# Kernel optimization log

Hardware: AMD Instinct MI355X
Metric: run time of the kernel (lower is better)

## Reference

```python
import jax, jax.numpy as jnp
import numpy as np

NUM_GROUP = 32
CHANNELS = 512
NUM_PER_GROUP = CHANNELS // NUM_GROUP  # 16
BN_EPS = 1e-5


def setup_inputs() -> dict:
    key = jax.random.key(0)
    k = jax.random.split(key, 5)
    B, C, W, H = 32, CHANNELS, 56, 56
    x = jax.random.normal(k[0], (B, C, W, H), dtype=jnp.float32)
    fc_w = jax.random.normal(k[1], (C, C), dtype=jnp.float32) / np.float32(np.sqrt(C))
    fc_b = jax.random.normal(k[2], (C,), dtype=jnp.float32) * 0.01
    bn_gamma = jnp.ones((C,), jnp.float32) + 0.1 * jax.random.normal(k[3], (C,), dtype=jnp.float32)
    bn_beta = 0.1 * jax.random.normal(k[4], (C,), dtype=jnp.float32)
    return {"x": x, "fc_w": fc_w, "fc_b": fc_b, "bn_gamma": bn_gamma, "bn_beta": bn_beta}


def reference(x, fc_w, fc_b, bn_gamma, bn_beta):
    b, c, w, h = x.shape
    G, P = NUM_GROUP, NUM_PER_GROUP
    # NHWC flatten -> [N, C], N = b*w*h
    t = x.transpose(0, 2, 3, 1).reshape(-1, c)
    t = t + (t @ fc_w.T + fc_b)                         # fc + residual
    t = t.reshape(-1, G, P)                             # [N, G, P]
    # bmm(t^T, t): [N, P, G] x [N, G, P] -> [N, P, P], then /32 and tanh
    s = jnp.tanh(jnp.einsum('ngp,ngq->npq', t, t) / 32.0)
    s = s.reshape(b, w, w, P * P)                       # requires w == h
    # F.interpolate(size=(w, c), mode='nearest') over last two dims:
    # dim-2 is w->w (identity); dim-3 is P*P -> c with src = floor(dst*in/out)
    idx = (jnp.arange(c) * (P * P)) // c
    s = s[..., idx]                                     # [b, w, w, c]
    s = s.transpose(0, 3, 1, 2)                         # [b, c, w, w]
    # BatchNorm2d, training-mode batch statistics (biased var), eps=1e-5
    mean = s.mean(axis=(0, 2, 3), keepdims=True)
    var = s.var(axis=(0, 2, 3), keepdims=True)
    s = (s - mean) * jax.lax.rsqrt(var + BN_EPS)
    s = s * bn_gamma[None, :, None, None] + bn_beta[None, :, None, None]
    return x + s
```

## Files before the change

kernel.cpp:

```cpp
#include <hip/hip_runtime.h>
#include <hip/hip_bf16.h>
#include <cstdint>

typedef __bf16 bf16x8 __attribute__((ext_vector_type(8)));
typedef unsigned short ushortx8 __attribute__((ext_vector_type(8)));
typedef unsigned short ushortx4 __attribute__((ext_vector_type(4)));
typedef float f32x4 __attribute__((ext_vector_type(4)));

constexpr int Cc  = 512;
constexpr int Ssp = 3136;
constexpr float NINV = 1.f / 100352.f;

__device__ __forceinline__ unsigned short f2bf(float f) {
    union { float f; unsigned u; } a; a.f = f;
    unsigned u = a.u;
    unsigned r = u + 0x7fffu + ((u >> 16) & 1u);
    return (unsigned short)(r >> 16);
}
__device__ __forceinline__ float bf2f(unsigned short h) {
    union { unsigned u; float f; } a; a.u = ((unsigned)h) << 16;
    return a.f;
}
__device__ __forceinline__ float tanh_fast(float u) {
    float e = __expf(2.f * u);
    return 1.f - 2.f / (e + 1.f);
}
__device__ __forceinline__ int swz(int row, int k) {
    return k ^ (((row >> 2) & 7) << 3);
}

__global__ void kWconv(const float* __restrict__ w, unsigned short* __restrict__ wb) {
    int i = (blockIdx.x * 256 + threadIdx.x) * 4;
    float4 v = *(const float4*)(w + i);
    ushortx4 o;
    o[0] = f2bf(v.x); o[1] = f2bf(v.y); o[2] = f2bf(v.z); o[3] = f2bf(v.w);
    *(ushortx4*)(wb + i) = o;
}

__global__ __launch_bounds__(512) void kA(
    const float* __restrict__ x, const unsigned short* __restrict__ wb,
    const float* __restrict__ fcb, float* __restrict__ sbuf,
    float* __restrict__ gstats)
{
    __shared__ __attribute__((aligned(16))) unsigned short xl[64 * 72];
    __shared__ __attribute__((aligned(16))) unsigned short tl[64 * 520];
    __shared__ float statsl[512];

    const int tid  = threadIdx.x;
    const int wave = tid >> 6;
    const int lane = tid & 63;
    const int lg   = lane >> 4;
    const int lm   = lane & 15;

    const int blk = blockIdx.x;
    const int b   = blk / 49;
    const int sc  = blk % 49;
    const float* xA = x + (size_t)b * Cc * Ssp + sc * 64;

    f32x4 acc[4][4];
#pragma unroll
    for (int mi = 0; mi < 4; ++mi)
#pragma unroll
        for (int ni = 0; ni < 4; ++ni) acc[mi][ni] = (f32x4){0.f, 0.f, 0.f, 0.f};

    float bias[4];
#pragma unroll
    for (int ni = 0; ni < 4; ++ni) bias[ni] = fcb[wave * 64 + ni * 16 + lm];

    const int stid = tid >> 4;
    const int s4   = (tid & 15) * 4;

    for (int kt = 0; kt < 8; ++kt) {
#pragma unroll
        for (int it = 0; it < 2; ++it) {
            int kr = stid + it * 32;
            float4 v = *(const float4*)(xA + (size_t)(kt * 64 + kr) * Ssp + s4);
#pragma unroll
            for (int i = 0; i < 4; ++i) {
                int row = s4 + i;
                xl[row * 72 + swz(row, kr)] = f2bf(((const float*)&v)[i]);
            }
        }
        __syncthreads();

        if (wave == kt) {
#pragma unroll
            for (int mi = 0; mi < 4; ++mi)
#pragma unroll
                for (int ni = 0; ni < 4; ++ni) {
                    int kl = ni * 16 + lm;
#pragma unroll
                    for (int j = 0; j < 4; ++j) {
                        int row = mi * 16 + lg * 4 + j;
                        acc[mi][ni][j] += bf2f(xl[row * 72 + swz(row, kl)]);
                    }
                }
        }

#pragma unroll
        for (int ks = 0; ks < 2; ++ks) {
            bf16x8 af[4], bfr[4];
#pragma unroll
            for (int mi = 0; mi < 4; ++mi) {
                int row = mi * 16 + lm;
                int k0  = swz(row, ks * 32 + 8 * lg);
                af[mi] = *(const bf16x8*)&xl[row * 72 + k0];
            }
#pragma unroll
            for (int ni = 0; ni < 4; ++ni) {
                int c = wave * 64 + ni * 16 + lm;
                bfr[ni] = *(const bf16x8*)(wb + (size_t)c * 512 + kt * 64 + ks * 32 + 8 * lg);
            }
#pragma unroll
            for (int mi = 0; mi < 4; ++mi)
#pragma unroll
                for (int ni = 0; ni < 4; ++ni)
                    acc[mi][ni] = __builtin_amdgcn_mfma_f32_16x16x32_bf16(
                        af[mi], bfr[ni], acc[mi][ni], 0, 0, 0);
        }
        __syncthreads();
    }

#pragma unroll
    for (int mi = 0; mi < 4; ++mi)
#pragma unroll
        for (int ni = 0; ni < 4; ++ni) {
            int c = wave * 64 + ni * 16 + lm;
#pragma unroll
            for (int j = 0; j < 4; ++j) {
                int srow = mi * 16 + lg * 4 + j;
                tl[srow * 520 + c] = f2bf(acc[mi][ni][j] + bias[ni]);
            }
        }
    statsl[tid] = 0.f;
    __syncthreads();

    float sum[4] = {0, 0, 0, 0}, ssq[4] = {0, 0, 0, 0};
    const size_t nbase = (size_t)b * Ssp + sc * 64;
    for (int nn = 0; nn < 8; ++nn) {
        int nl = wave * 8 + nn;
        ushortx8 uf;
#pragma unroll
        for (int bs = 0; bs < 8; ++bs) {
            int cidx = (bs * 4 + lg) * 16 + lm;
            uf[bs] = tl[nl * 520 + cidx];
        }
        bf16x8 f = __builtin_bit_cast(bf16x8, uf);
        f32x4 d = __builtin_amdgcn_mfma_f32_16x16x32_bf16(f, f, (f32x4){0, 0, 0, 0}, 0, 0, 0);
        float* sp = sbuf + (nbase + nl) * 256;
#pragma unroll
        for (int j = 0; j < 4; ++j) {
            float sv = tanh_fast(d[j] * (1.f / 32.f));
            sum[j] += sv; ssq[j] += sv * sv;
            sp[(lg * 4 + j) * 16 + lm] = sv;
        }
    }
#pragma unroll
    for (int j = 0; j < 4; ++j) {
        int pq = (lg * 4 + j) * 16 + lm;
        atomicAdd(&statsl[pq], sum[j]);
        atomicAdd(&statsl[256 + pq], ssq[j]);
    }
    __syncthreads();
    if (tid < 256) {
        atomicAdd(&gstats[tid], statsl[tid]);
        atomicAdd(&gstats[256 + tid], statsl[256 + tid]);
    }
}

__global__ void kB(const float* __restrict__ gstats, float* __restrict__ minv) {
    int t = threadIdx.x;
    float mean = gstats[t] * NINV;
    float var  = gstats[256 + t] * NINV - mean * mean;
    minv[t]       = mean;
    minv[256 + t] = rsqrtf(var + 1e-5f);
}

__global__ __launch_bounds__(256) void kC(
    const float* __restrict__ x, const float* __restrict__ sbuf,
    const float* __restrict__ minv, const float* __restrict__ gamma,
    const float* __restrict__ beta, float* __restrict__ out)
{
    __shared__ __attribute__((aligned(16))) float sl[32 * 260];
    const int tid = threadIdx.x;
    const int blk = blockIdx.x;
    const int b = blk / 98, sc = blk % 98;

    const float* sb = sbuf + ((size_t)b * Ssp + sc * 32) * 256;
#pragma unroll
    for (int i = 0; i < 8; ++i) {
        int flat = (i * 256 + tid) * 4;
        float4 v = *(const float4*)(sb + flat);
        int n = flat >> 8, pq = flat & 255;
        *(float4*)&sl[n * 260 + pq] = v;
    }
    __syncthreads();

    const size_t xoff = (size_t)b * Cc * Ssp + sc * 32;
    const float* xb = x + xoff;
    float* ob = out + xoff;
    for (int iter = 0; iter < 16; ++iter) {
        int task = iter * 256 + tid;
        int c  = task >> 3;
        int s4 = (task & 7) * 4;
        int pq = c >> 1;
        float m = minv[pq], inv = minv[256 + pq];
        float ga = gamma[c] * inv;
        float be = beta[c] - m * ga;
        float4 xv = *(const float4*)(xb + (size_t)c * Ssp + s4);
        float4 r;
        r.x = xv.x + sl[(s4 + 0) * 260 + pq] * ga + be;
        r.y = xv.y + sl[(s4 + 1) * 260 + pq] * ga + be;
        r.z = xv.z + sl[(s4 + 2) * 260 + pq] * ga + be;
        r.w = xv.w + sl[(s4 + 3) * 260 + pq] * ga + be;
        *(float4*)(ob + (size_t)c * Ssp + s4) = r;
    }
}

extern "C" void kernel_launch(void* const* d_in, const int* in_sizes, int n_in,
                              void* d_out, int out_size, void* d_ws, size_t ws_size,
                              hipStream_t stream) {
    const float* x     = (const float*)d_in[0];
    const float* fcw   = (const float*)d_in[1];
    const float* fcb   = (const float*)d_in[2];
    const float* gamma = (const float*)d_in[3];
    const float* beta  = (const float*)d_in[4];
    float* out = (float*)d_out;

    char* ws = (char*)d_ws;
    unsigned short* wb = (unsigned short*)ws;
    float* gstats = (float*)(ws + 512 * 512 * 2);
    float* minv   = (float*)(ws + 512 * 512 * 2 + 2048);
    float* sbuf   = (float*)(ws + (1 << 20));

    hipMemsetAsync(gstats, 0, 2048, stream);
    kWconv<<<dim3(256), dim3(256), 0, stream>>>(fcw, wb);
    kA<<<dim3(1568), dim3(512), 0, stream>>>(x, wb, fcb, sbuf, gstats);
    kB<<<dim3(1), dim3(256), 0, stream>>>(gstats, minv);
    kC<<<dim3(3136), dim3(256), 0, stream>>>(x, sbuf, minv, gamma, beta, out);
}
```

Before: 596.1 us.

## Store tanh intermediate as fp16 channel-major and prefetch x tiles in fc GEMM

The intermediate tanh scores are packed to fp16 and written in a [pq][N] layout through an LDS transpose, which halves intermediate traffic and lets the final kernel read one contiguous row per (batch, channel) block. The fc GEMM loop now register-prefetches the next x tile, hoists the weight fragment loads, and uses raw barriers with an occupancy hint. The final kernel becomes a simple per-channel streaming pass. fp16 storage adds rounding error to the normalized scores.

```diff
diff --git a/kernel.cpp b/kernel.cpp
--- a/kernel.cpp
+++ b/kernel.cpp
@@ -1,5 +1,6 @@
 #include <hip/hip_runtime.h>
 #include <hip/hip_bf16.h>
+#include <hip/hip_fp16.h>
 #include <cstdint>
 
 typedef __bf16 bf16x8 __attribute__((ext_vector_type(8)));
@@ -20,6 +21,13 @@
 __device__ __forceinline__ float bf2f(unsigned short h) {
     union { unsigned u; float f; } a; a.u = ((unsigned)h) << 16;
     return a.f;
+}
+__device__ __forceinline__ unsigned short f2h(float f) {
+    _Float16 h = (_Float16)f;
+    return __builtin_bit_cast(unsigned short, h);
+}
+__device__ __forceinline__ float h2f(unsigned short u) {
+    return (float)__builtin_bit_cast(_Float16, u);
 }
 __device__ __forceinline__ float tanh_fast(float u) {
     float e = __expf(2.f * u);
@@ -37,9 +45,9 @@
     *(ushortx4*)(wb + i) = o;
 }
 
-__global__ __launch_bounds__(512) void kA(
+__global__ __launch_bounds__(512, 4) void kA(
     const float* __restrict__ x, const unsigned short* __restrict__ wb,
-    const float* __restrict__ fcb, float* __restrict__ sbuf,
+    const float* __restrict__ fcb, unsigned short* __restrict__ sb16,
     float* __restrict__ gstats)
 {
     __shared__ __attribute__((aligned(16))) unsigned short xl[64 * 72];
@@ -70,18 +78,32 @@
     const int stid = tid >> 4;
     const int s4   = (tid & 15) * 4;
 
+    float4 xv0 = *(const float4*)(xA + (size_t)stid * Ssp + s4);
+    float4 xv1 = *(const float4*)(xA + (size_t)(stid + 32) * Ssp + s4);
+
+#pragma unroll
     for (int kt = 0; kt < 8; ++kt) {
-#pragma unroll
-        for (int it = 0; it < 2; ++it) {
-            int kr = stid + it * 32;
-            float4 v = *(const float4*)(xA + (size_t)(kt * 64 + kr) * Ssp + s4);
-#pragma unroll
-            for (int i = 0; i < 4; ++i) {
-                int row = s4 + i;
-                xl[row * 72 + swz(row, kr)] = f2bf(((const float*)&v)[i]);
+        __builtin_amdgcn_s_barrier();
+#pragma unroll
+        for (int i = 0; i < 4; ++i) {
+            int row = s4 + i;
+            xl[row * 72 + swz(row, stid)]      = f2bf(((const float*)&xv0)[i]);
+            xl[row * 72 + swz(row, stid + 32)] = f2bf(((const float*)&xv1)[i]);
+        }
+        if (kt < 7) {
+            xv0 = *(const float4*)(xA + (size_t)((kt + 1) * 64 + stid) * Ssp + s4);
+            xv1 = *(const float4*)(xA + (size_t)((kt + 1) * 64 + stid + 32) * Ssp + s4);
+        }
+        bf16x8 wv[8];
+#pragma unroll
+        for (int ks = 0; ks < 2; ++ks)
+#pragma unroll
+            for (int ni = 0; ni < 4; ++ni) {
+                int c = wave * 64 + ni * 16 + lm;
+                wv[ks * 4 + ni] = *(const bf16x8*)(wb + (size_t)c * 512 + kt * 64 + ks * 32 + 8 * lg);
             }
-        }
-        __syncthreads();
+        asm volatile("s_waitcnt lgkmcnt(0)" ::: "memory");
+        __builtin_amdgcn_s_barrier();
 
         if (wave == kt) {
 #pragma unroll
@@ -99,26 +121,16 @@
 
 #pragma unroll
         for (int ks = 0; ks < 2; ++ks) {
-            bf16x8 af[4], bfr[4];
 #pragma unroll
             for (int mi = 0; mi < 4; ++mi) {
                 int row = mi * 16 + lm;
-                int k0  = swz(row, ks * 32 + 8 * lg);
-                af[mi] = *(const bf16x8*)&xl[row * 72 + k0];
-            }
-#pragma unroll
-            for (int ni = 0; ni < 4; ++ni) {
-                int c = wave * 64 + ni * 16 + lm;
-                bfr[ni] = *(const bf16x8*)(wb + (size_t)c * 512 + kt * 64 + ks * 32 + 8 * lg);
-            }
-#pragma unroll
-            for (int mi = 0; mi < 4; ++mi)
+                bf16x8 af = *(const bf16x8*)&xl[row * 72 + swz(row, ks * 32 + 8 * lg)];
 #pragma unroll
                 for (int ni = 0; ni < 4; ++ni)
                     acc[mi][ni] = __builtin_amdgcn_mfma_f32_16x16x32_bf16(
-                        af[mi], bfr[ni], acc[mi][ni], 0, 0, 0);
-        }
-        __syncthreads();
+                        af, wv[ks * 4 + ni], acc[mi][ni], 0, 0, 0);
+            }
+        }
     }
 
 #pragma unroll
@@ -136,7 +148,7 @@
     __syncthreads();
 
     float sum[4] = {0, 0, 0, 0}, ssq[4] = {0, 0, 0, 0};
-    const size_t nbase = (size_t)b * Ssp + sc * 64;
+    unsigned svp[8][2];
     for (int nn = 0; nn < 8; ++nn) {
         int nl = wave * 8 + nn;
         ushortx8 uf;
@@ -147,13 +159,15 @@
         }
         bf16x8 f = __builtin_bit_cast(bf16x8, uf);
         f32x4 d = __builtin_amdgcn_mfma_f32_16x16x32_bf16(f, f, (f32x4){0, 0, 0, 0}, 0, 0, 0);
-        float* sp = sbuf + (nbase + nl) * 256;
+        unsigned short h[4];
 #pragma unroll
         for (int j = 0; j < 4; ++j) {
             float sv = tanh_fast(d[j] * (1.f / 32.f));
             sum[j] += sv; ssq[j] += sv * sv;
-            sp[(lg * 4 + j) * 16 + lm] = sv;
-        }
+            h[j] = f2h(sv);
+        }
+        svp[nn][0] = (unsigned)h[0] | ((unsigned)h[1] << 16);
+        svp[nn][1] = (unsigned)h[2] | ((unsigned)h[3] << 16);
     }
 #pragma unroll
     for (int j = 0; j < 4; ++j) {
@@ -165,6 +179,26 @@
     if (tid < 256) {
         atomicAdd(&gstats[tid], statsl[tid]);
         atomicAdd(&gstats[256 + tid], statsl[256 + tid]);
+    }
+
+    const size_t nbase = (size_t)b * Ssp + sc * 64;
+#pragma unroll
+    for (int ci = 0; ci < 4; ++ci) {
+        __syncthreads();
+        if (lg == ci) {
+#pragma unroll
+            for (int nn = 0; nn < 8; ++nn)
+#pragma unroll
+                for (int j = 0; j < 4; ++j) {
+                    unsigned short hv = (unsigned short)(svp[nn][j >> 1] >> (16 * (j & 1)));
+                    xl[(j * 16 + lm) * 72 + wave * 8 + nn] = hv;
+                }
+        }
+        __syncthreads();
+        int pql = tid >> 3;
+        int n8  = (tid & 7) * 8;
+        ushortx8 v = *(const ushortx8*)&xl[pql * 72 + n8];
+        *(ushortx8*)(sb16 + (size_t)(ci * 64 + pql) * 100352 + nbase + n8) = v;
     }
 }
 
@@ -177,43 +211,33 @@
 }
 
 __global__ __launch_bounds__(256) void kC(
-    const float* __restrict__ x, const float* __restrict__ sbuf,
+    const float* __restrict__ x, const unsigned short* __restrict__ sb16,
     const float* __restrict__ minv, const float* __restrict__ gamma,
     const float* __restrict__ beta, float* __restrict__ out)
 {
-    __shared__ __attribute__((aligned(16))) float sl[32 * 260];
-    const int tid = threadIdx.x;
-    const int blk = blockIdx.x;
-    const int b = blk / 98, sc = blk % 98;
-
-    const float* sb = sbuf + ((size_t)b * Ssp + sc * 32) * 256;
-#pragma unroll
-    for (int i = 0; i < 8; ++i) {
-        int flat = (i * 256 + tid) * 4;
-        float4 v = *(const float4*)(sb + flat);
-        int n = flat >> 8, pq = flat & 255;
-        *(float4*)&sl[n * 260 + pq] = v;
-    }
-    __syncthreads();
-
-    const size_t xoff = (size_t)b * Cc * Ssp + sc * 32;
-    const float* xb = x + xoff;
-    float* ob = out + xoff;
-    for (int iter = 0; iter < 16; ++iter) {
-        int task = iter * 256 + tid;
-        int c  = task >> 3;
-        int s4 = (task & 7) * 4;
-        int pq = c >> 1;
-        float m = minv[pq], inv = minv[256 + pq];
-        float ga = gamma[c] * inv;
-        float be = beta[c] - m * ga;
-        float4 xv = *(const float4*)(xb + (size_t)c * Ssp + s4);
-        float4 r;
-        r.x = xv.x + sl[(s4 + 0) * 260 + pq] * ga + be;
-        r.y = xv.y + sl[(s4 + 1) * 260 + pq] * ga + be;
-        r.z = xv.z + sl[(s4 + 2) * 260 + pq] * ga + be;
-        r.w = xv.w + sl[(s4 + 3) * 260 + pq] * ga + be;
-        *(float4*)(ob + (size_t)c * Ssp + s4) = r;
+    const int bc = blockIdx.x;
+    const int b = bc >> 9, c = bc & 511;
+    const int pq = c >> 1;
+    const float m = minv[pq], inv = minv[256 + pq];
+    const float ga = gamma[c] * inv;
+    const float be = beta[c] - m * ga;
+    const float* xb = x + ((size_t)b * Cc + c) * Ssp;
+    float* ob = out + ((size_t)b * Cc + c) * Ssp;
+    const unsigned short* sr = sb16 + (size_t)pq * 100352 + (size_t)b * Ssp;
+    const int t = threadIdx.x;
+#pragma unroll
+    for (int i = 0; i < 4; ++i) {
+        int idx = i * 256 + t;
+        if (idx < 784) {
+            float4 xv = *(const float4*)(xb + idx * 4);
+            ushortx4 sv = *(const ushortx4*)(sr + idx * 4);
+            float4 r;
+            r.x = xv.x + h2f(sv[0]) * ga + be;
+            r.y = xv.y + h2f(sv[1]) * ga + be;
+            r.z = xv.z + h2f(sv[2]) * ga + be;
+            r.w = xv.w + h2f(sv[3]) * ga + be;
+            *(float4*)(ob + idx * 4) = r;
+        }
     }
 }
 
@@ -231,11 +255,11 @@
     unsigned short* wb = (unsigned short*)ws;
     float* gstats = (float*)(ws + 512 * 512 * 2);
     float* minv   = (float*)(ws + 512 * 512 * 2 + 2048);
-    float* sbuf   = (float*)(ws + (1 << 20));
+    unsigned short* sb16 = (unsigned short*)(ws + (1 << 20));
 
     hipMemsetAsync(gstats, 0, 2048, stream);
     kWconv<<<dim3(256), dim3(256), 0, stream>>>(fcw, wb);
-    kA<<<dim3(1568), dim3(512), 0, stream>>>(x, wb, fcb, sbuf, gstats);
+    kA<<<dim3(1568), dim3(512), 0, stream>>>(x, wb, fcb, sb16, gstats);
     kB<<<dim3(1), dim3(256), 0, stream>>>(gstats, minv);
-    kC<<<dim3(3136), dim3(256), 0, stream>>>(x, sbuf, minv, gamma, beta, out);
-}
+    kC<<<dim3(16384), dim3(256), 0, stream>>>(x, sb16, minv, gamma, beta, out);
+}
```

Result: slower. 702.0 us (+17.8%).
